# Kernel tuning notes

Hardware: AMD Instinct MI355X
Metric: run time of the kernel (lower is better)

The kernel has to match this reference:

```python
import jax, jax.numpy as jnp
import numpy as np

CUTOFF = 6.0   # matches init cutoff
D = 32         # descriptor/MLP width
NTYPES = 3     # len(type_map)


def setup_inputs() -> dict:
    key = jax.random.key(0)
    ks = jax.random.split(key, 13)
    b, n, m, n_ghost = 2, 8192, 64, 512
    neighbor_vectors = jax.random.normal(ks[0], (b, n, m, 4), jnp.float32)
    element_map = jax.random.randint(ks[1], (b, n), 0, NTYPES, jnp.int32)
    central_atoms = jax.random.randint(ks[2], (b, n), 0, n, jnp.int32)
    neighbor_indices = jax.random.randint(ks[3], (b, n, m), 0, n + n_ghost, jnp.int32)
    neighbor_types = jax.random.randint(ks[4], (b, n, m), 0, NTYPES, jnp.int32)
    type_embed = 0.1 * jax.random.normal(ks[5], (NTYPES, D), jnp.float32)
    elem_bias = 0.1 * jax.random.normal(ks[6], (NTYPES,), jnp.float32)
    W1 = 0.5 * jax.random.normal(ks[7], (4, D), jnp.float32)
    b1 = 0.1 * jax.random.normal(ks[8], (D,), jnp.float32)
    W2 = (1.0 / np.sqrt(D)) * jax.random.normal(ks[9], (D, D), jnp.float32)
    b2 = 0.1 * jax.random.normal(ks[10], (D,), jnp.float32)
    W3 = (1.0 / np.sqrt(D)) * jax.random.normal(ks[11], (D, 1), jnp.float32)
    b3 = 0.1 * jax.random.normal(ks[12], (1,), jnp.float32)
    return dict(element_map=element_map, central_atoms=central_atoms,
                neighbor_indices=neighbor_indices, neighbor_types=neighbor_types,
                neighbor_vectors=neighbor_vectors, n_ghost=n_ghost,
                type_embed=type_embed, elem_bias=elem_bias,
                W1=W1, b1=b1, W2=W2, b2=b2, W3=W3, b3=b3)


def _field_Ei(rel, element_map, neighbor_types, type_embed, elem_bias, W1, b1, W2, b2, W3, b3):
    # rel: [b,n,m,3] relative positions; recompute distance as the torch forward does
    dist = jnp.linalg.norm(rel, axis=-1, keepdims=True)                 # [b,n,m,1]
    fc = 0.5 * (jnp.cos(jnp.pi * jnp.minimum(dist, CUTOFF) / CUTOFF) + 1.0)
    s = jnp.exp(-dist) * fc                                             # smooth radial weight
    feat = jnp.concatenate([s, s * rel], axis=-1)                       # [b,n,m,4]
    h = jnp.tanh(feat @ W1 + b1 + type_embed[neighbor_types])           # [b,n,m,D]
    g = h.mean(axis=2)                                                  # pool over neighbors -> [b,n,D]
    h2 = jnp.tanh(g @ W2 + b2)                                          # [b,n,D]
    Ei = h2 @ W3 + b3 + elem_bias[element_map][..., None]               # [b,n,1]
    return Ei


def derive_mechanics(grad_Ei, neighbor_vectors, neighbor_indices, n_ghost):
    # grad_Ei: [b,n,m,3] = d(sum Ei)/d r_ij, with r_ij = r_j - r_i
    b, n, m, _ = grad_Ei.shape
    ntot = n + n_ghost
    bidx = jnp.arange(b)[:, None, None]
    # force on central atom i: +sum_j dE/dr_ij ; reaction scattered to neighbor j: -dE/dr_ij
    force = jnp.zeros((b, ntot, 3), grad_Ei.dtype)
    force = force.at[:, :n].add(grad_Ei.sum(axis=2))
    force = force.at[bidx, neighbor_indices].add(-grad_Ei)
    rij = neighbor_vectors[..., 1:]                                     # [b,n,m,3]
    pv = (rij[..., :, None] * grad_Ei[..., None, :]).reshape(b, n, m, 9)  # pair virial r (x) dE
    virial = pv.sum(axis=(1, 2))                                        # [b,9]
    av = jnp.zeros((b, ntot, 9), grad_Ei.dtype)
    av = av.at[bidx, neighbor_indices].add(pv)
    return force[:, :n], virial, av[:, :n]


def reference(element_map, central_atoms, neighbor_indices, neighbor_types,
              neighbor_vectors, n_ghost, type_embed, elem_bias,
              W1, b1, W2, b2, W3, b3):
    rel = neighbor_vectors[..., 1:]                                     # [b,n,m,3]

    def ei_sum(r):
        Ei = _field_Ei(r, element_map, neighbor_types, type_embed, elem_bias,
                       W1, b1, W2, b2, W3, b3)
        return Ei.sum(), Ei

    grad_Ei, Ei = jax.grad(ei_sum, has_aux=True)(rel)                   # matches autograd.grad w/ ones mask
    Etot = Ei.sum(axis=1)                                               # [b,1]
    dist = jnp.linalg.norm(rel, axis=-1, keepdims=True)
    nv = jnp.concatenate([dist, rel], axis=-1)
    force, virial, atomic_virial = derive_mechanics(grad_Ei, nv, neighbor_indices, n_ghost)
    return Etot, Ei, force, virial, atomic_virial
```

## Files before the change

### kernel.cpp

```cpp
#include <hip/hip_runtime.h>

#define CUTOFF_F 6.0f
#define PI_F 3.14159265358979323846f
#define CAP 112

typedef __fp16 fp16x2 __attribute__((ext_vector_type(2)));

__device__ __forceinline__ unsigned pk2(float a, float b) {
  union { fp16x2 h; unsigned u; } cv;
  cv.h = __builtin_amdgcn_cvt_pkrtz(a, b);
  return cv.u;
}
__device__ __forceinline__ float f16bits(unsigned v) {
  union { unsigned short u; __fp16 h; } cv; cv.u = (unsigned short)v; return (float)cv.h;
}

template<int CTRL>
__device__ __forceinline__ float dpp_add(float x) {
  int y = __builtin_amdgcn_update_dpp(0, __float_as_int(x), CTRL, 0xf, 0xf, true);
  return x + __int_as_float(y);
}
__device__ __forceinline__ float wave_sum63(float x) {
  x = dpp_add<0x111>(x);
  x = dpp_add<0x112>(x);
  x = dpp_add<0x114>(x);
  x = dpp_add<0x118>(x);
  x = dpp_add<0x142>(x);
  x = dpp_add<0x143>(x);
  return x;
}

__device__ __forceinline__ float fast_tanh(float x) {
  float e = __expf(2.0f * x);
  return 1.0f - 2.0f * __builtin_amdgcn_rcpf(e + 1.0f);
}

__global__ __launch_bounds__(256) void field_main(
    const int* __restrict__ element_map,
    const int* __restrict__ neighbor_indices,
    const int* __restrict__ neighbor_types,
    const float4* __restrict__ neighbor_vectors,
    const float* __restrict__ type_embed,
    const float* __restrict__ elem_bias,
    const float* __restrict__ W1,
    const float* __restrict__ b1,
    const float* __restrict__ W2,
    const float* __restrict__ b2,
    const float* __restrict__ W3,
    const float* __restrict__ b3,
    float* __restrict__ outEi,
    float* __restrict__ outForce,
    float* __restrict__ outAV,
    int* __restrict__ counts,
    float4* __restrict__ bucket,
    float* __restrict__ partials,
    int n)
{
  __shared__ float4 sW1t[32];
  __shared__ float  sbte[3][32];
  __shared__ float  sW2[32 * 33];
  __shared__ float  sW3[32];
  __shared__ float  sb2[32];
  __shared__ float  sElemBias[3];
  __shared__ float  sb3;
  __shared__ float  blkEi[4];
  __shared__ float  blkVir[4][9];
  __shared__ unsigned hbuf[4][64][17];
  __shared__ float    gtd[4][3][32];

  const int tid = threadIdx.x;

  if (tid < 32) {
    sW1t[tid] = make_float4(W1[tid], W1[32 + tid], W1[64 + tid], W1[96 + tid]);
    sW3[tid]  = W3[tid];
    sb2[tid]  = b2[tid];
  } else if (tid < 128) {
    int t = (tid - 32) >> 5, k = tid & 31;
    sbte[t][k] = b1[k] + type_embed[t * 32 + k];
  } else if (tid == 128) {
    sb3 = b3[0];
  } else if (tid < 132) {
    sElemBias[tid - 129] = elem_bias[tid - 129];
  }
  for (int i = tid; i < 1024; i += 256) {
    int l = i >> 5, k = i & 31;
    sW2[l * 33 + k] = W2[i];
  }
  __syncthreads();

  const int wave = tid >> 6;
  const int lane = tid & 63;
  const int atom = blockIdx.x * 4 + wave;
  const int bb = atom / n;
  const int ii = atom - bb * n;

  const int base = atom * 64 + lane;
  const int idx = neighbor_indices[base];
  const int dest = bb * n + idx;

  int pos = 0;
  const bool real = (idx < n);
  if (real) pos = atomicAdd(&counts[dest], 1);

  const float4 nv = neighbor_vectors[base];
  const float rx = nv.y, ry = nv.z, rz = nv.w;
  const int typ = neighbor_types[base];

  const float d2 = rx * rx + ry * ry + rz * rz;
  const float d = sqrtf(d2);
  const float invd = (d > 0.0f) ? __builtin_amdgcn_rcpf(d) : 0.0f;
  float s, sp;
  if (d < CUTOFF_F) {
    const float arg = d * (PI_F / CUTOFF_F);
    const float cs = __cosf(arg);
    const float sn = __sinf(arg);
    const float e = __expf(-d);
    const float fc = 0.5f * (cs + 1.0f);
    const float fcp = -(0.5f * PI_F / CUTOFF_F) * sn;
    s = e * fc;
    sp = e * (fcp - fc);
  } else {
    s = 0.0f;
    sp = 0.0f;
  }
  const float f1 = s * rx, f2 = s * ry, f3 = s * rz;

  float h[32];
#pragma unroll
  for (int k = 0; k < 32; k += 2) {
    const float4 wa = sW1t[k];
    float pa = sbte[typ][k];
    pa = fmaf(s, wa.x, pa); pa = fmaf(f1, wa.y, pa);
    pa = fmaf(f2, wa.z, pa); pa = fmaf(f3, wa.w, pa);
    h[k] = fast_tanh(pa);
    const float4 wb = sW1t[k + 1];
    float pb = sbte[typ][k + 1];
    pb = fmaf(s, wb.x, pb); pb = fmaf(f1, wb.y, pb);
    pb = fmaf(f2, wb.z, pb); pb = fmaf(f3, wb.w, pb);
    h[k + 1] = fast_tanh(pb);
    hbuf[wave][lane][k >> 1] = pk2(h[k], h[k + 1]);
  }

  const int halfid = lane >> 5;
  const int kd = lane & 31;
  const int dw = kd >> 1;
  const int sh = (kd & 1) << 4;
  float gsum = 0.0f;
#pragma unroll
  for (int j = 0; j < 32; ++j) {
    const unsigned w = hbuf[wave][j + (halfid << 5)][dw];
    gsum += f16bits(w >> sh);
  }
  gsum += __shfl_xor(gsum, 32);
  const float gk = gsum * (1.0f / 64.0f);
  if (halfid == 0) gtd[wave][0][kd] = gk;

  __builtin_amdgcn_s_waitcnt(0);

  float acc = sb2[kd];
#pragma unroll
  for (int l = 0; l < 32; l += 4) {
    const float4 g4 = *(const float4*)&gtd[wave][0][l];
    acc = fmaf(g4.x, sW2[(l + 0) * 33 + kd], acc);
    acc = fmaf(g4.y, sW2[(l + 1) * 33 + kd], acc);
    acc = fmaf(g4.z, sW2[(l + 2) * 33 + kd], acc);
    acc = fmaf(g4.w, sW2[(l + 3) * 33 + kd], acc);
  }
  const float h2 = fast_tanh(acc);
  const float tl = (1.0f - h2 * h2) * sW3[kd];
  if (halfid == 0) gtd[wave][1][kd] = tl;

  float dgacc = 0.0f;
#pragma unroll
  for (int l = 0; l < 32; l += 4) {
    const float4 t4 = *(const float4*)&gtd[wave][1][l];
    dgacc = fmaf(t4.x, sW2[kd * 33 + l + 0], dgacc);
    dgacc = fmaf(t4.y, sW2[kd * 33 + l + 1], dgacc);
    dgacc = fmaf(t4.z, sW2[kd * 33 + l + 2], dgacc);
    dgacc = fmaf(t4.w, sW2[kd * 33 + l + 3], dgacc);
  }
  if (halfid == 0) gtd[wave][2][kd] = dgacc * (1.0f / 64.0f);

  float p = h2 * sW3[kd];

  float q0 = 0.0f, q1 = 0.0f, q2 = 0.0f, q3 = 0.0f;
#pragma unroll
  for (int k = 0; k < 32; k += 4) {
    const float4 d4 = *(const float4*)&gtd[wave][2][k];
#pragma unroll
    for (int u = 0; u < 4; ++u) {
      const float dgk = (u == 0) ? d4.x : (u == 1) ? d4.y : (u == 2) ? d4.z : d4.w;
      const float hk = h[k + u];
      const float dpre = dgk * (1.0f - hk * hk);
      const float4 w = sW1t[k + u];
      q0 = fmaf(dpre, w.x, q0);
      q1 = fmaf(dpre, w.y, q1);
      q2 = fmaf(dpre, w.z, q2);
      q3 = fmaf(dpre, w.w, q3);
    }
  }

  const float common = sp * invd * (q0 + q1 * rx + q2 * ry + q3 * rz);
  const float gx = fmaf(common, rx, s * q1);
  const float gy = fmaf(common, ry, s * q2);
  const float gz = fmaf(common, rz, s * q3);

  if (real) {
    if (pos < CAP) {
      float4 pay;
      pay.x = __uint_as_float(pk2(gx, gy));
      pay.y = __uint_as_float(pk2(gz, rx));
      pay.z = __uint_as_float(pk2(ry, rz));
      pay.w = 0.0f;
      bucket[(size_t)dest * CAP + pos] = pay;
    } else {
      float* fdst = outForce + (size_t)dest * 3;
      atomicAdd(fdst + 0, -gx);
      atomicAdd(fdst + 1, -gy);
      atomicAdd(fdst + 2, -gz);
      float* adst = outAV + (size_t)dest * 9;
      atomicAdd(adst + 0, rx * gx); atomicAdd(adst + 1, rx * gy); atomicAdd(adst + 2, rx * gz);
      atomicAdd(adst + 3, ry * gx); atomicAdd(adst + 4, ry * gy); atomicAdd(adst + 5, ry * gz);
      atomicAdd(adst + 6, rz * gx); atomicAdd(adst + 7, rz * gy); atomicAdd(adst + 8, rz * gz);
    }
  }

  float sfx = wave_sum63(gx);
  float sfy = wave_sum63(gy);
  float sfz = wave_sum63(gz);
  float vr0 = wave_sum63(rx * gx), vr1 = wave_sum63(rx * gy), vr2 = wave_sum63(rx * gz);
  float vr3 = wave_sum63(ry * gx), vr4 = wave_sum63(ry * gy), vr5 = wave_sum63(ry * gz);
  float vr6 = wave_sum63(rz * gx), vr7 = wave_sum63(rz * gy), vr8 = wave_sum63(rz * gz);
  float psum = wave_sum63(p) * 0.5f;

  if (lane == 63) {
    const int em = element_map[atom];
    const float Ei_val = psum + sb3 + sElemBias[em];
    outEi[atom] = Ei_val;
    blkEi[wave] = Ei_val;
    blkVir[wave][0] = vr0; blkVir[wave][1] = vr1; blkVir[wave][2] = vr2;
    blkVir[wave][3] = vr3; blkVir[wave][4] = vr4; blkVir[wave][5] = vr5;
    blkVir[wave][6] = vr6; blkVir[wave][7] = vr7; blkVir[wave][8] = vr8;
    float* fdst = outForce + (size_t)atom * 3;
    fdst[0] = sfx; fdst[1] = sfy; fdst[2] = sfz;
  }

  __syncthreads();
  if (tid < 9) {
    partials[blockIdx.x * 10 + tid] =
        blkVir[0][tid] + blkVir[1][tid] + blkVir[2][tid] + blkVir[3][tid];
  } else if (tid == 9) {
    partials[blockIdx.x * 10 + 9] = blkEi[0] + blkEi[1] + blkEi[2] + blkEi[3];
  }
}

__global__ __launch_bounds__(256) void field_gather(
    const int* __restrict__ counts,
    const float4* __restrict__ bucket,
    float* __restrict__ outForce,
    float* __restrict__ outAV,
    int n)
{
  const int tid = threadIdx.x;
  const int wave = tid >> 6;
  const int lane = tid & 63;
  const int dest = blockIdx.x * 4 + wave;

  int cnt = counts[dest];
  if (cnt > CAP) cnt = CAP;

  float fx = 0.0f, fy = 0.0f, fz = 0.0f;
  float a0 = 0, a1 = 0, a2 = 0, a3 = 0, a4 = 0, a5 = 0, a6 = 0, a7 = 0, a8 = 0;

#pragma unroll 2
  for (int l = lane; l < cnt; l += 64) {
    const float4 pay = bucket[(size_t)dest * CAP + l];
    const unsigned w0 = __float_as_uint(pay.x);
    const unsigned w1 = __float_as_uint(pay.y);
    const unsigned w2 = __float_as_uint(pay.z);
    const float gx = f16bits(w0), gy = f16bits(w0 >> 16);
    const float gz = f16bits(w1), rx = f16bits(w1 >> 16);
    const float ry = f16bits(w2), rz = f16bits(w2 >> 16);
    fx -= gx; fy -= gy; fz -= gz;
    a0 = fmaf(rx, gx, a0); a1 = fmaf(rx, gy, a1); a2 = fmaf(rx, gz, a2);
    a3 = fmaf(ry, gx, a3); a4 = fmaf(ry, gy, a4); a5 = fmaf(ry, gz, a5);
    a6 = fmaf(rz, gx, a6); a7 = fmaf(rz, gy, a7); a8 = fmaf(rz, gz, a8);
  }

  fx = wave_sum63(fx); fy = wave_sum63(fy); fz = wave_sum63(fz);
  a0 = wave_sum63(a0); a1 = wave_sum63(a1); a2 = wave_sum63(a2);
  a3 = wave_sum63(a3); a4 = wave_sum63(a4); a5 = wave_sum63(a5);
  a6 = wave_sum63(a6); a7 = wave_sum63(a7); a8 = wave_sum63(a8);

  if (lane == 63) {
    float* f = outForce + (size_t)dest * 3;
    f[0] += fx; f[1] += fy; f[2] += fz;
    float* a = outAV + (size_t)dest * 9;
    a[0] += a0; a[1] += a1; a[2] += a2;
    a[3] += a3; a[4] += a4; a[5] += a5;
    a[6] += a6; a[7] += a7; a[8] += a8;
  }
}

__global__ __launch_bounds__(256) void field_reduce(
    const float* __restrict__ partials,
    float* __restrict__ outEtot,
    float* __restrict__ outVirial,
    int half)
{
  __shared__ float sacc[4][10];
  const int b = blockIdx.x;
  const int tid = threadIdx.x;
  const int lane = tid & 63;
  const int wave = tid >> 6;

  float acc[10] = {0, 0, 0, 0, 0, 0, 0, 0, 0, 0};
  for (int r = b * half + tid; r < (b + 1) * half; r += 256) {
#pragma unroll
    for (int t = 0; t < 10; ++t) acc[t] += partials[r * 10 + t];
  }
#pragma unroll
  for (int t = 0; t < 10; ++t) acc[t] = wave_sum63(acc[t]);
  if (lane == 63) {
#pragma unroll
    for (int t = 0; t < 10; ++t) sacc[wave][t] = acc[t];
  }
  __syncthreads();
  if (tid < 9) {
    outVirial[b * 9 + tid] = sacc[0][tid] + sacc[1][tid] + sacc[2][tid] + sacc[3][tid];
  } else if (tid == 9) {
    outEtot[b] = sacc[0][9] + sacc[1][9] + sacc[2][9] + sacc[3][9];
  }
}

extern "C" void kernel_launch(void* const* d_in, const int* in_sizes, int n_in,
                              void* d_out, int out_size, void* d_ws, size_t ws_size,
                              hipStream_t stream) {
  const int* element_map        = (const int*)d_in[0];
  const int* neighbor_indices   = (const int*)d_in[2];
  const int* neighbor_types     = (const int*)d_in[3];
  const float4* neighbor_vectors = (const float4*)d_in[4];
  const float* type_embed = (const float*)d_in[6];
  const float* elem_bias  = (const float*)d_in[7];
  const float* W1 = (const float*)d_in[8];
  const float* b1 = (const float*)d_in[9];
  const float* W2 = (const float*)d_in[10];
  const float* b2 = (const float*)d_in[11];
  const float* W3 = (const float*)d_in[12];
  const float* b3 = (const float*)d_in[13];

  const int B = 2;
  const int bn = in_sizes[0];
  const int n = bn / B;
  const int nblk = bn / 4;

  float* out = (float*)d_out;
  float* outEtot   = out;
  float* outEi     = outEtot + B;
  float* outForce  = outEi + bn;
  float* outVirial = outForce + (size_t)bn * 3;
  float* outAV     = outVirial + (size_t)B * 9;

  char* ws = (char*)d_ws;
  int* counts = (int*)ws;
  size_t countBytes = (size_t)bn * sizeof(int);
  float* partials = (float*)(ws + countBytes);
  size_t partialBytes = (size_t)nblk * 10 * sizeof(float);
  float4* bucket = (float4*)(ws + countBytes + partialBytes);

  (void)hipMemsetAsync(d_out, 0, (size_t)out_size * sizeof(float), stream);
  (void)hipMemsetAsync(counts, 0, countBytes, stream);

  dim3 grid(nblk), block(256);
  hipLaunchKernelGGL(field_main, grid, block, 0, stream,
                     element_map, neighbor_indices, neighbor_types,
                     neighbor_vectors, type_embed, elem_bias,
                     W1, b1, W2, b2, W3, b3,
                     outEi, outForce, outAV,
                     counts, bucket, partials, n);
  hipLaunchKernelGGL(field_gather, grid, block, 0, stream,
                     counts, bucket, outForce, outAV, n);
  hipLaunchKernelGGL(field_reduce, dim3(B), block, 0, stream,
                     partials, outEtot, outVirial, nblk / B);
}
```

Baseline: 153.5 us.

## Route self-force through buckets and drop full output memset with coalesced gather stores

The self-force term now goes into the per-destination bucket (or a 12-float overflow buffer) instead of being written straight to the output. That lets the gather kernel own every force and atomic-virial value and write them with plain coalesced stores through shared memory. The full memset of the output buffer is replaced by a smaller memset of counts plus the overflow buffer. It also removes an explicit waitcnt and hoists the element_map load. The risks are that the self force is now stored in fp16, which loses precision, and the bucket gains one extra entry per atom.

```diff
diff --git a/kernel.cpp b/kernel.cpp
--- a/kernel.cpp
+++ b/kernel.cpp
@@ -49,9 +49,8 @@
     const float* __restrict__ W3,
     const float* __restrict__ b3,
     float* __restrict__ outEi,
-    float* __restrict__ outForce,
-    float* __restrict__ outAV,
     int* __restrict__ counts,
+    float* __restrict__ obuf,
     float4* __restrict__ bucket,
     float* __restrict__ partials,
     int n)
@@ -92,11 +91,11 @@
   const int lane = tid & 63;
   const int atom = blockIdx.x * 4 + wave;
   const int bb = atom / n;
-  const int ii = atom - bb * n;
 
   const int base = atom * 64 + lane;
   const int idx = neighbor_indices[base];
   const int dest = bb * n + idx;
+  const int em = element_map[atom];
 
   int pos = 0;
   const bool real = (idx < n);
@@ -155,8 +154,6 @@
   const float gk = gsum * (1.0f / 64.0f);
   if (halfid == 0) gtd[wave][0][kd] = gk;
 
-  __builtin_amdgcn_s_waitcnt(0);
-
   float acc = sb2[kd];
 #pragma unroll
   for (int l = 0; l < 32; l += 4) {
@@ -214,14 +211,11 @@
       pay.w = 0.0f;
       bucket[(size_t)dest * CAP + pos] = pay;
     } else {
-      float* fdst = outForce + (size_t)dest * 3;
-      atomicAdd(fdst + 0, -gx);
-      atomicAdd(fdst + 1, -gy);
-      atomicAdd(fdst + 2, -gz);
-      float* adst = outAV + (size_t)dest * 9;
-      atomicAdd(adst + 0, rx * gx); atomicAdd(adst + 1, rx * gy); atomicAdd(adst + 2, rx * gz);
-      atomicAdd(adst + 3, ry * gx); atomicAdd(adst + 4, ry * gy); atomicAdd(adst + 5, ry * gz);
-      atomicAdd(adst + 6, rz * gx); atomicAdd(adst + 7, rz * gy); atomicAdd(adst + 8, rz * gz);
+      float* ob = obuf + (size_t)dest * 12;
+      atomicAdd(ob + 0, -gx); atomicAdd(ob + 1, -gy); atomicAdd(ob + 2, -gz);
+      atomicAdd(ob + 3, rx * gx); atomicAdd(ob + 4, rx * gy); atomicAdd(ob + 5, rx * gz);
+      atomicAdd(ob + 6, ry * gx); atomicAdd(ob + 7, ry * gy); atomicAdd(ob + 8, ry * gz);
+      atomicAdd(ob + 9, rz * gx); atomicAdd(ob + 10, rz * gy); atomicAdd(ob + 11, rz * gz);
     }
   }
 
@@ -234,15 +228,24 @@
   float psum = wave_sum63(p) * 0.5f;
 
   if (lane == 63) {
-    const int em = element_map[atom];
     const float Ei_val = psum + sb3 + sElemBias[em];
     outEi[atom] = Ei_val;
     blkEi[wave] = Ei_val;
     blkVir[wave][0] = vr0; blkVir[wave][1] = vr1; blkVir[wave][2] = vr2;
     blkVir[wave][3] = vr3; blkVir[wave][4] = vr4; blkVir[wave][5] = vr5;
     blkVir[wave][6] = vr6; blkVir[wave][7] = vr7; blkVir[wave][8] = vr8;
-    float* fdst = outForce + (size_t)atom * 3;
-    fdst[0] = sfx; fdst[1] = sfy; fdst[2] = sfz;
+    const int spos = atomicAdd(&counts[atom], 1);
+    if (spos < CAP) {
+      float4 pay;
+      pay.x = __uint_as_float(pk2(-sfx, -sfy));
+      pay.y = __uint_as_float(pk2(-sfz, 0.0f));
+      pay.z = 0.0f;
+      pay.w = 0.0f;
+      bucket[(size_t)atom * CAP + spos] = pay;
+    } else {
+      float* ob = obuf + (size_t)atom * 12;
+      atomicAdd(ob + 0, sfx); atomicAdd(ob + 1, sfy); atomicAdd(ob + 2, sfz);
+    }
   }
 
   __syncthreads();
@@ -257,17 +260,19 @@
 __global__ __launch_bounds__(256) void field_gather(
     const int* __restrict__ counts,
     const float4* __restrict__ bucket,
+    const float* __restrict__ obuf,
     float* __restrict__ outForce,
     float* __restrict__ outAV,
     int n)
 {
+  __shared__ float sf[4][12];
   const int tid = threadIdx.x;
   const int wave = tid >> 6;
   const int lane = tid & 63;
   const int dest = blockIdx.x * 4 + wave;
 
-  int cnt = counts[dest];
-  if (cnt > CAP) cnt = CAP;
+  const int rawcnt = counts[dest];
+  const int cnt = (rawcnt > CAP) ? CAP : rawcnt;
 
   float fx = 0.0f, fy = 0.0f, fz = 0.0f;
   float a0 = 0, a1 = 0, a2 = 0, a3 = 0, a4 = 0, a5 = 0, a6 = 0, a7 = 0, a8 = 0;
@@ -293,12 +298,26 @@
   a6 = wave_sum63(a6); a7 = wave_sum63(a7); a8 = wave_sum63(a8);
 
   if (lane == 63) {
-    float* f = outForce + (size_t)dest * 3;
-    f[0] += fx; f[1] += fy; f[2] += fz;
-    float* a = outAV + (size_t)dest * 9;
-    a[0] += a0; a[1] += a1; a[2] += a2;
-    a[3] += a3; a[4] += a4; a[5] += a5;
-    a[6] += a6; a[7] += a7; a[8] += a8;
+    if (rawcnt > CAP) {
+      const float* ob = obuf + (size_t)dest * 12;
+      fx += ob[0]; fy += ob[1]; fz += ob[2];
+      a0 += ob[3]; a1 += ob[4]; a2 += ob[5];
+      a3 += ob[6]; a4 += ob[7]; a5 += ob[8];
+      a6 += ob[9]; a7 += ob[10]; a8 += ob[11];
+    }
+    sf[wave][0] = fx; sf[wave][1] = fy; sf[wave][2] = fz;
+    sf[wave][3] = a0; sf[wave][4] = a1; sf[wave][5] = a2;
+    sf[wave][6] = a3; sf[wave][7] = a4; sf[wave][8] = a5;
+    sf[wave][9] = a6; sf[wave][10] = a7; sf[wave][11] = a8;
+  }
+  __syncthreads();
+
+  const int d0 = blockIdx.x * 4;
+  if (tid < 12) {
+    outForce[(size_t)d0 * 3 + tid] = sf[tid / 3][tid % 3];
+  } else if (tid >= 64 && tid < 100) {
+    const int t = tid - 64;
+    outAV[(size_t)d0 * 9 + t] = sf[t / 9][3 + t % 9];
   }
 }
 
@@ -364,22 +383,22 @@
   char* ws = (char*)d_ws;
   int* counts = (int*)ws;
   size_t countBytes = (size_t)bn * sizeof(int);
-  float* partials = (float*)(ws + countBytes);
+  float* obuf = (float*)(ws + countBytes);
+  size_t obufBytes = (size_t)bn * 12 * sizeof(float);
+  float* partials = (float*)(ws + countBytes + obufBytes);
   size_t partialBytes = (size_t)nblk * 10 * sizeof(float);
-  float4* bucket = (float4*)(ws + countBytes + partialBytes);
-
-  (void)hipMemsetAsync(d_out, 0, (size_t)out_size * sizeof(float), stream);
-  (void)hipMemsetAsync(counts, 0, countBytes, stream);
+  float4* bucket = (float4*)(ws + countBytes + obufBytes + partialBytes);
+
+  (void)hipMemsetAsync(counts, 0, countBytes + obufBytes, stream);
 
   dim3 grid(nblk), block(256);
   hipLaunchKernelGGL(field_main, grid, block, 0, stream,
                      element_map, neighbor_indices, neighbor_types,
                      neighbor_vectors, type_embed, elem_bias,
                      W1, b1, W2, b2, W3, b3,
-                     outEi, outForce, outAV,
-                     counts, bucket, partials, n);
+                     outEi, counts, obuf, bucket, partials, n);
   hipLaunchKernelGGL(field_gather, grid, block, 0, stream,
-                     counts, bucket, outForce, outAV, n);
+                     counts, bucket, obuf, outForce, outAV, n);
   hipLaunchKernelGGL(field_reduce, dim3(B), block, 0, stream,
                      partials, outEtot, outVirial, nblk / B);
 }
```

Result: no change. 151.6 us (-1.3%).
